# Optimization experiments

Measured on AMD Instinct MI355X. Metric: run time of the kernel, lower is better.

Reference implementation:

```python
import jax, jax.numpy as jnp
import numpy as np

B = 512          # number of (query, corpus) pairs
MAX_SET = 128    # max_set_size
D_IN, E_IN = 32, 16
D = 128          # node_state_dim == filters_3
E_ENC = 64
M_HID = 256
T_DIM = 128      # transform_dim
N_PROP = 5
SINKHORN_ITERS = 20
TEMP = 0.1
DEG = 8


def setup_inputs() -> dict:
    key = jax.random.key(0)
    ks = jax.random.split(key, 16)
    # alternating graph sizes: query 128/64, corpus 64/128
    qsizes = np.where(np.arange(B) % 2 == 0, 128, 64).astype(np.int32)
    csizes = np.where(np.arange(B) % 2 == 0, 64, 128).astype(np.int32)
    sizes_flat = np.stack([qsizes, csizes], 1).reshape(-1)        # [2B] interleaved q,c
    N = int(sizes_flat.sum())                                     # 98304
    E = DEG * N                                                   # 786432
    starts = np.concatenate([[0], np.cumsum(sizes_flat)[:-1]])
    graph_idx = np.repeat(np.arange(2 * B), sizes_flat).astype(np.int32)
    rng = np.random.default_rng(0)
    from_idx = rng.integers(0, N, E).astype(np.int64)
    g = graph_idx[from_idx]                                       # keep edges within a graph
    to_idx = (starts[g] + rng.integers(0, 1 << 30, E) % sizes_flat[g]).astype(np.int64)

    def W(k, shape):
        s = 1.0 / np.sqrt(shape[0])
        return jax.random.uniform(k, shape, jnp.float32, -s, s)

    return dict(
        node_features=jax.random.normal(ks[0], (N, D_IN), jnp.float32),
        edge_features=jax.random.normal(ks[1], (E, E_IN), jnp.float32),
        enc_node_w=W(ks[2], (D_IN, D)), enc_node_b=jnp.zeros((D,), jnp.float32),
        enc_edge_w=W(ks[3], (E_IN, E_ENC)), enc_edge_b=jnp.zeros((E_ENC,), jnp.float32),
        msg_w1=W(ks[4], (2 * D + E_ENC, M_HID)), msg_b1=jnp.zeros((M_HID,), jnp.float32),
        msg_w2=W(ks[5], (M_HID, D)), msg_b2=jnp.zeros((D,), jnp.float32),
        rmsg_w1=W(ks[6], (2 * D + E_ENC, M_HID)), rmsg_b1=jnp.zeros((M_HID,), jnp.float32),
        rmsg_w2=W(ks[7], (M_HID, D)), rmsg_b2=jnp.zeros((D,), jnp.float32),
        upd_w1=W(ks[8], (2 * D, M_HID)), upd_b1=jnp.zeros((M_HID,), jnp.float32),
        upd_w2=W(ks[9], (M_HID, D)), upd_b2=jnp.zeros((D,), jnp.float32),
        fc1_w=W(ks[10], (D, T_DIM)), fc1_b=jnp.zeros((T_DIM,), jnp.float32),
        fc2_w=W(ks[11], (T_DIM, T_DIM)), fc2_b=jnp.zeros((T_DIM,), jnp.float32),
        from_idx=jnp.asarray(from_idx, jnp.int32),
        to_idx=jnp.asarray(to_idx, jnp.int32),
        graph_idx=jnp.asarray(graph_idx, jnp.int32),
        qsizes=jnp.asarray(qsizes, jnp.int32),
        csizes=jnp.asarray(csizes, jnp.int32),
    )


def _mlp2(x, w1, b1, w2, b2):
    return jax.nn.relu(x @ w1 + b1) @ w2 + b2


def reference(node_features, edge_features, enc_node_w, enc_node_b, enc_edge_w, enc_edge_b,
              msg_w1, msg_b1, msg_w2, msg_b2, rmsg_w1, rmsg_b1, rmsg_w2, rmsg_b2,
              upd_w1, upd_b1, upd_w2, upd_b2, fc1_w, fc1_b, fc2_w, fc2_b,
              from_idx, to_idx, graph_idx, qsizes, csizes):
    N = node_features.shape[0]
    # GraphEncoder: linear MLPs on node / edge features
    h = node_features @ enc_node_w + enc_node_b                   # [N, D]
    e = edge_features @ enc_edge_w + enc_edge_b                   # [E, E_ENC]
    # GraphPropLayer applied n_prop_layers times (shared params)
    for _ in range(N_PROP):
        src, dst = h[from_idx], h[to_idx]
        m = _mlp2(jnp.concatenate([src, dst, e], -1), msg_w1, msg_b1, msg_w2, msg_b2)
        agg = jax.ops.segment_sum(m, to_idx, num_segments=N)
        mr = _mlp2(jnp.concatenate([dst, src, e], -1), rmsg_w1, rmsg_b1, rmsg_w2, rmsg_b2)
        agg = agg + jax.ops.segment_sum(mr, from_idx, num_segments=N)
        h = h + _mlp2(jnp.concatenate([agg, h], -1), upd_w1, upd_b1, upd_w2, upd_b2)
    # split into per-graph chunks and pad to MAX_SET (scatter by (pair, side, position))
    sizes_flat = jnp.stack([qsizes, csizes], 1).reshape(-1)       # [2B]
    starts = jnp.concatenate([jnp.zeros((1,), sizes_flat.dtype), jnp.cumsum(sizes_flat)[:-1]])
    pos = jnp.arange(N, dtype=jnp.int32) - starts[graph_idx]
    pair, side = graph_idx // 2, graph_idx % 2
    stacked = jnp.zeros((B, 2, MAX_SET, D), h.dtype).at[pair, side, pos].set(h)
    stacked_q, stacked_c = stacked[:, 0], stacked[:, 1]           # [B, MAX_SET, D]
    # masked transform
    tq = _mlp2(stacked_q, fc1_w, fc1_b, fc2_w, fc2_b)
    tc = _mlp2(stacked_c, fc1_w, fc1_b, fc2_w, fc2_b)
    ar = jnp.arange(MAX_SET)
    qmask = (ar[None, :] < qsizes[:, None]).astype(h.dtype)[:, :, None]
    cmask = (ar[None, :] < csizes[:, None]).astype(h.dtype)[:, :, None]
    mq, mc = qmask * tq, cmask * tc
    # sinkhorn (noise_factor = 0, temperature = 0.1, 20 iters)
    log_alpha = jnp.einsum('bqd,bcd->bqc', mq, mc) / TEMP         # [B, MAX_SET, MAX_SET]
    for _ in range(SINKHORN_ITERS):
        log_alpha = log_alpha - jax.scipy.special.logsumexp(log_alpha, axis=2, keepdims=True)
        log_alpha = log_alpha - jax.scipy.special.logsumexp(log_alpha, axis=1, keepdims=True)
    plan = jnp.exp(log_alpha)
    # masked residual score
    scores = -jnp.sum(jax.nn.relu(stacked_q - plan @ stacked_c), axis=(1, 2))  # [B]
    return scores
```

## Files before the change

### kernel.cpp

```cpp
#include <hip/hip_runtime.h>

using bf16x8 = __attribute__((ext_vector_type(8))) __bf16;
using u16x8  = __attribute__((ext_vector_type(8))) unsigned short;
using f32x4  = __attribute__((ext_vector_type(4))) float;
using f32x2  = __attribute__((ext_vector_type(2))) float;

#define DEV static __device__ __forceinline__

constexpr int NN = 98304;
constexpr int NE = 786432;
constexpr int NB = 512;

constexpr size_t OFF_HB  = 0;
constexpr size_t OFF_AGG = OFF_HB + (size_t)NN*128*2;
constexpr size_t OFF_TH  = OFF_AGG;
constexpr size_t OFF_TL  = OFF_AGG + (size_t)NN*128*2;
constexpr size_t OFF_W   = OFF_AGG + (size_t)NN*128*4;

constexpr size_t WO_W1TM = 0;
constexpr size_t WO_W1TR = WO_W1TM + (size_t)81920*2;
constexpr size_t WO_W2TM = WO_W1TR + (size_t)81920*2;
constexpr size_t WO_W2TR = WO_W2TM + (size_t)32768*2;
constexpr size_t WO_W1TU = WO_W2TR + (size_t)32768*2;
constexpr size_t WO_W2TU = WO_W1TU + (size_t)65536*2;
constexpr size_t WO_WNT  = WO_W2TU + (size_t)32768*2;
constexpr size_t WO_WETP = WO_WNT  + (size_t)4096*2;
constexpr size_t WO_FC1F = WO_WETP + (size_t)2048*2;
constexpr size_t WO_FC2F = WO_FC1F + (size_t)16384*4;
constexpr size_t WO_BNF  = WO_FC2F + (size_t)16384*4;
constexpr size_t WO_BEF  = WO_BNF + 128*4;
constexpr size_t WO_B1M  = WO_BEF + 64*4;
constexpr size_t WO_B2M  = WO_B1M + 256*4;
constexpr size_t WO_B1R  = WO_B2M + 128*4;
constexpr size_t WO_B2R  = WO_B1R + 256*4;
constexpr size_t WO_B1U  = WO_B2R + 128*4;
constexpr size_t WO_B2U  = WO_B1U + 256*4;
constexpr size_t WO_FC1B = WO_B2U + 128*4;
constexpr size_t WO_FC2B = WO_FC1B + 128*4;
constexpr size_t WO_FLAG = WO_FC2B + 128*4;
constexpr size_t WO_END  = WO_FLAG + 16;

constexpr size_t OFF_HL  = OFF_W + WO_END;
constexpr size_t WS_MINI = OFF_HL;
constexpr size_t WS_FULL = OFF_HL + (size_t)NN*128*2;

constexpr int    SCAN_CHUNKS= NN/256;
constexpr size_t CSR_INTS   = (size_t)2*(NN+1) + (size_t)2*NN + (size_t)2*NE + 768;
constexpr size_t CSR_BYTES  = CSR_INTS*4;
constexpr size_t WS_FULL_G  = WS_FULL + CSR_BYTES;
constexpr size_t WS_MINI_G  = WS_MINI + CSR_BYTES;

DEV unsigned short f2bf(float f){
  unsigned u = __float_as_uint(f);
  u += 0x7fffu + ((u >> 16) & 1u);
  return (unsigned short)(u >> 16);
}
DEV float bf2f(unsigned short s){ return __uint_as_float(((unsigned)s) << 16); }

DEV unsigned short ldbf(const void* p, size_t i, int fl){
  return fl ? ((const unsigned short*)p)[i] : f2bf(((const float*)p)[i]);
}
DEV float ldf(const void* p, size_t i, int fl){
  return fl ? bf2f(((const unsigned short*)p)[i]) : ((const float*)p)[i];
}

DEV f32x4 mfma16(u16x8 a, u16x8 b, f32x4 c){
  bf16x8 A, B;
  __builtin_memcpy(&A, &a, 16);
  __builtin_memcpy(&B, &b, 16);
  return __builtin_amdgcn_mfma_f32_16x16x32_bf16(A, B, c, 0, 0, 0);
}

__global__ void k_dtype(const unsigned short* nf_u16, int* flag){
  if (threadIdx.x != 0 || blockIdx.x != 0) return;
  int sane = 0;
  for (int i = 0; i < 64; ++i){
    unsigned short v = nf_u16[2*i];
    int e = (v >> 7) & 0xFF;
    if (e >= 0x70 && e <= 0x8E) sane++;
  }
  *flag = (sane >= 32) ? 1 : 0;
}

__global__ void k_sent(float* out){
  int i = blockIdx.x*256 + threadIdx.x;
  if (i < NB) out[i] = 10000.f;
}

__global__ void k_canary(void* out, const int* flag){
  int i = blockIdx.x*256 + threadIdx.x;
  if (i < NB){
    if (*flag) ((unsigned short*)out)[i] = (unsigned short)0x4580u;
    else       ((float*)out)[i] = 4096.f;
  }
}

__global__ void k_zero(float* agg){
  f32x4* p = (f32x4*)agg;
  int gtid = blockIdx.x*256 + threadIdx.x;
  for (int i = gtid; i < NN*128/4; i += 786432){
    f32x4 z = {0.f, 0.f, 0.f, 0.f};
    p[i] = z;
  }
}

__global__ void k_prep(
  const void* enc_node_w, const void* enc_node_b,
  const void* enc_edge_w, const void* enc_edge_b,
  const void* msg_w1, const void* msg_b1,
  const void* msg_w2, const void* msg_b2,
  const void* rmsg_w1, const void* rmsg_b1,
  const void* rmsg_w2, const void* rmsg_b2,
  const void* upd_w1, const void* upd_b1,
  const void* upd_w2, const void* upd_b2,
  const void* fc1_w, const void* fc1_b,
  const void* fc2_w, const void* fc2_b,
  char* wsb)
{
  int fl = *(const int*)(wsb + OFF_W + WO_FLAG);
  int i = blockIdx.x*256 + threadIdx.x;
  unsigned short* W1Tm = (unsigned short*)(wsb + OFF_W + WO_W1TM);
  unsigned short* W1Tr = (unsigned short*)(wsb + OFF_W + WO_W1TR);
  unsigned short* W2Tm = (unsigned short*)(wsb + OFF_W + WO_W2TM);
  unsigned short* W2Tr = (unsigned short*)(wsb + OFF_W + WO_W2TR);
  unsigned short* W1Tu = (unsigned short*)(wsb + OFF_W + WO_W1TU);
  unsigned short* W2Tu = (unsigned short*)(wsb + OFF_W + WO_W2TU);
  unsigned short* WnT  = (unsigned short*)(wsb + OFF_W + WO_WNT);
  unsigned short* WeTp = (unsigned short*)(wsb + OFF_W + WO_WETP);
  float* fc1f = (float*)(wsb + OFF_W + WO_FC1F);
  float* fc2f = (float*)(wsb + OFF_W + WO_FC2F);
  float* bnf  = (float*)(wsb + OFF_W + WO_BNF);
  float* bef  = (float*)(wsb + OFF_W + WO_BEF);
  float* b1m  = (float*)(wsb + OFF_W + WO_B1M);
  float* b2m  = (float*)(wsb + OFF_W + WO_B2M);
  float* b1r  = (float*)(wsb + OFF_W + WO_B1R);
  float* b2r  = (float*)(wsb + OFF_W + WO_B2R);
  float* b1u  = (float*)(wsb + OFF_W + WO_B1U);
  float* b2u  = (float*)(wsb + OFF_W + WO_B2U);
  float* f1b  = (float*)(wsb + OFF_W + WO_FC1B);
  float* f2b  = (float*)(wsb + OFF_W + WO_FC2B);

  if (i < 81920){ W1Tm[i] = ldbf(msg_w1,  (size_t)(i%320)*256 + (i/320), fl); return; } i -= 81920;
  if (i < 81920){ W1Tr[i] = ldbf(rmsg_w1, (size_t)(i%320)*256 + (i/320), fl); return; } i -= 81920;
  if (i < 32768){ W2Tm[i] = ldbf(msg_w2,  (size_t)(i%256)*128 + (i/256), fl); return; } i -= 32768;
  if (i < 32768){ W2Tr[i] = ldbf(rmsg_w2, (size_t)(i%256)*128 + (i/256), fl); return; } i -= 32768;
  if (i < 65536){ W1Tu[i] = ldbf(upd_w1,  (size_t)(i%256)*256 + (i/256), fl); return; } i -= 65536;
  if (i < 32768){ W2Tu[i] = ldbf(upd_w2,  (size_t)(i%256)*128 + (i/256), fl); return; } i -= 32768;
  if (i <  4096){ WnT[i]  = ldbf(enc_node_w, (size_t)(i%32)*128 + (i/32), fl); return; } i -= 4096;
  if (i <  2048){ int k = i%32, n = i/32;
                  WeTp[i] = (k<16) ? ldbf(enc_edge_w, (size_t)k*64 + n, fl) : (unsigned short)0; return; } i -= 2048;
  if (i < 16384){ fc1f[i] = ldf(fc1_w, i, fl); return; } i -= 16384;
  if (i < 16384){ fc2f[i] = ldf(fc2_w, i, fl); return; } i -= 16384;
  if (i <   128){ bnf[i] = ldf(enc_node_b, i, fl); return; } i -= 128;
  if (i <    64){ bef[i] = ldf(enc_edge_b, i, fl); return; } i -= 64;
  if (i <   256){ b1m[i] = ldf(msg_b1, i, fl); return; } i -= 256;
  if (i <   128){ b2m[i] = ldf(msg_b2, i, fl); return; } i -= 128;
  if (i <   256){ b1r[i] = ldf(rmsg_b1, i, fl); return; } i -= 256;
  if (i <   128){ b2r[i] = ldf(rmsg_b2, i, fl); return; } i -= 128;
  if (i <   256){ b1u[i] = ldf(upd_b1, i, fl); return; } i -= 256;
  if (i <   128){ b2u[i] = ldf(upd_b2, i, fl); return; } i -= 128;
  if (i <   128){ f1b[i] = ldf(fc1_b, i, fl); return; } i -= 128;
  if (i <   128){ f2b[i] = ldf(fc2_b, i, fl); return; }
}

__global__ void k_csr_zero(int* cur0, int* cur1){
  int i = blockIdx.x*256 + threadIdx.x;
  if (i < NN){ cur0[i] = 0; cur1[i] = 0; }
}
__global__ void k_csr_count(const int* from_idx, const int* to_idx, int* cur0, int* cur1){
  int e = blockIdx.x*256 + threadIdx.x;
  if (e < NE){
    atomicAdd(&cur0[to_idx[e]], 1);
    atomicAdd(&cur1[from_idx[e]], 1);
  }
}
__global__ void k_scan1(const int* cur0, const int* cur1, int* csum){
  __shared__ int red[256];
  int b = blockIdx.x, tid = threadIdx.x;
  const int* c = (b >= SCAN_CHUNKS) ? cur1 : cur0;
  int cb = (b >= SCAN_CHUNKS) ? (b - SCAN_CHUNKS) : b;
  red[tid] = c[cb*256 + tid];
  __syncthreads();
  for (int off = 128; off > 0; off >>= 1){
    if (tid < off) red[tid] += red[tid + off];
    __syncthreads();
  }
  if (tid == 0) csum[b] = red[0];
}
__global__ void k_scan2(int* csum, int* offs0, int* offs1){
  int wv = threadIdx.x >> 6, lane = threadIdx.x & 63;
  if (wv >= 2) return;
  int basei = wv * SCAN_CHUNKS;
  int carry = 0;
  for (int j = 0; j < SCAN_CHUNKS/64; ++j){
    int x = csum[basei + j*64 + lane];
    int s = x;
    for (int off = 1; off < 64; off <<= 1){
      int t = __shfl_up(s, off, 64);
      if (lane >= off) s += t;
    }
    csum[basei + j*64 + lane] = s - x + carry;
    carry += __shfl(s, 63, 64);
  }
  if (lane == 0){
    if (wv == 0) offs0[NN] = carry; else offs1[NN] = carry;
  }
}
__global__ void k_scan3(int* cur0, int* cur1, const int* csum, int* offs0, int* offs1){
  __shared__ int s[256];
  int b = blockIdx.x, tid = threadIdx.x;
  int dir = (b >= SCAN_CHUNKS) ? 1 : 0;
  int cb  = dir ? (b - SCAN_CHUNKS) : b;
  int* c    = dir ? cur1 : cur0;
  int* offs = dir ? offs1 : offs0;
  int v = c[cb*256 + tid];
  s[tid] = v;
  __syncthreads();
  for (int off = 1; off < 256; off <<= 1){
    int t = (tid >= off) ? s[tid - off] : 0;
    __syncthreads();
    s[tid] += t;
    __syncthreads();
  }
  int excl = s[tid] - v + csum[b];
  offs[cb*256 + tid] = excl;
  c[cb*256 + tid] = excl;
}
__global__ void k_csr_fill(const int* from_idx, const int* to_idx,
                           int* cur0, int* cur1, int* ent0, int* ent1){
  int e = blockIdx.x*256 + threadIdx.x;
  if (e < NE){
    int p0 = atomicAdd(&cur0[to_idx[e]], 1);   ent0[p0] = e;
    int p1 = atomicAdd(&cur1[from_idx[e]], 1); ent1[p1] = e;
  }
}

__global__ void __launch_bounds__(256) k_enc_node(
  const void* nf, const unsigned short* wnt, const float* bnf,
  unsigned short* hb, unsigned short* hl, int has_hl, const int* flag)
{
  int fl = *flag;
  const u16x8* wnt8 = (const u16x8*)wnt;
  int tid = threadIdx.x, wv = tid>>6, lane = tid&63, quad = lane>>4, l15 = lane&15;
  int n0 = blockIdx.x*64;
  f32x4 acc[4][2];
  for (int a=0;a<4;a++){ f32x4 z = {0.f,0.f,0.f,0.f}; acc[a][0]=z; acc[a][1]=z; }
  u16x8 av[4], bv[2];
  if (fl){
    const u16x8* nf8 = (const u16x8*)nf;
    for (int mt=0; mt<4; ++mt) av[mt] = nf8[(size_t)(n0 + mt*16 + l15)*4 + quad];
  } else {
    const float* nff = (const float*)nf;
    for (int mt=0; mt<4; ++mt){
      const float* rp = nff + (size_t)(n0 + mt*16 + l15)*32 + quad*8;
      u16x8 v;
      for (int j=0;j<8;j++) v[j] = f2bf(rp[j]);
      av[mt] = v;
    }
  }
  for (int nt=0; nt<2; ++nt) bv[nt] = wnt8[(size_t)(wv*32 + nt*16 + l15)*4 + quad];
  for (int mt=0; mt<4; ++mt)
    for (int nt=0; nt<2; ++nt)
      acc[mt][nt] = mfma16(av[mt], bv[nt], acc[mt][nt]);
  for (int mt=0; mt<4; ++mt)
    for (int nt=0; nt<2; ++nt){
      int n = wv*32 + nt*16 + l15;
      float bias = bnf[n];
      for (int r=0;r<4;r++){
        int m = mt*16 + quad*4 + r;
        float v = acc[mt][nt][r] + bias;
        size_t idx = (size_t)(n0+m)*128 + n;
        unsigned short hi = f2bf(v);
        hb[idx] = hi;
        if (has_hl) hl[idx] = f2bf(v - bf2f(hi));
      }
    }
}

__global__ void __launch_bounds__(256) k_msg(
  const unsigned short* hbg, const void* efg,
  const int* from_idx, const int* to_idx,
  const unsigned short* w1tm, const unsigned short* w1tr,
  const unsigned short* w2tm, const unsigned short* w2tr,
  const unsigned short* wetp, const float* bef,
  const float* b1m, const float* b2m, const float* b1r, const float* b2r,
  float* agg, const int* flag)
{
  __shared__ __align__(16) unsigned short XsB[40*32*8];
  __shared__ __align__(16) unsigned short HsB[32*32*8];
  __shared__ int fromS[32], toS[32];
  int fl = *flag;
  u16x8* Xs = (u16x8*)XsB;
  u16x8* Hs = (u16x8*)HsB;
  const u16x8* hb8   = (const u16x8*)hbg;
  const u16x8* wetp8 = (const u16x8*)wetp;
  const u16x8* w1tm8 = (const u16x8*)w1tm;
  const u16x8* w1tr8 = (const u16x8*)w1tr;
  const u16x8* w2tm8 = (const u16x8*)w2tm;
  const u16x8* w2tr8 = (const u16x8*)w2tr;

  int tid = threadIdx.x;
  int e0 = blockIdx.x*32;
  if (tid < 32) fromS[tid] = from_idx[e0 + tid];
  else if (tid < 64) toS[tid-32] = to_idx[e0 + tid - 32];
  __syncthreads();
  int m = tid & 31, g = tid >> 5;
  int wv = tid>>6, lane = tid&63, quad = lane>>4, l15 = lane&15;
  u16x8 zero8 = {0,0,0,0,0,0,0,0};

  for (int j=0; j<4; ++j){
    int kb = g + 8*j;
    u16x8 v = (kb < 16) ? hb8[(size_t)fromS[m]*16 + kb]
                        : hb8[(size_t)toS[m]*16 + (kb-16)];
    Xs[kb*32 + m] = v;
  }
  {
    f32x4 accE[2];
    for (int a=0;a<2;a++){ f32x4 z = {0.f,0.f,0.f,0.f}; accE[a]=z; }
    u16x8 bvE = wetp8[(size_t)(wv*16 + l15)*4 + quad];
    for (int mt=0; mt<2; ++mt){
      u16x8 avE = zero8;
      if (quad < 2){
        if (fl){
          avE = ((const u16x8*)efg)[(size_t)(e0 + mt*16 + l15)*2 + quad];
        } else {
          const float* ep = (const float*)efg + (size_t)(e0 + mt*16 + l15)*16 + quad*8;
          u16x8 v;
          for (int j=0;j<8;j++) v[j] = f2bf(ep[j]);
          avE = v;
        }
      }
      accE[mt] = mfma16(avE, bvE, accE[mt]);
    }
    int n = wv*16 + l15;
    float bias = bef[n];
    for (int mt=0; mt<2; ++mt)
      for (int r=0;r<4;r++){
        int me = mt*16 + quad*4 + r;
        XsB[((32 + (n>>3))*32 + me)*8 + (n&7)] = f2bf(accE[mt][r] + bias);
      }
  }
  __syncthreads();

  for (int dir=0; dir<2; ++dir){
    const u16x8* W1T = dir ? w1tr8 : w1tm8;
    const u16x8* W2T = dir ? w2tr8 : w2tm8;
    const float* B1  = dir ? b1r : b1m;
    const float* B2  = dir ? b2r : b2m;
    f32x4 acc1[2][4];
    for (int a=0;a<2;a++)
      for (int b=0;b<4;b++){ f32x4 z = {0.f,0.f,0.f,0.f}; acc1[a][b]=z; }
    for (int ks=0; ks<10; ++ks){
      u16x8 bv[4], av[2];
      for (int nt=0; nt<4; ++nt)
        bv[nt] = W1T[(size_t)(wv*64 + nt*16 + l15)*40 + ks*4 + quad];
      int kb = ks*4 + quad;
      int kbm = dir ? (kb < 32 ? (kb ^ 16) : kb) : kb;
      for (int mt=0; mt<2; ++mt)
        av[mt] = Xs[kbm*32 + mt*16 + l15];
      for (int mt=0; mt<2; ++mt)
        for (int nt=0; nt<4; ++nt)
          acc1[mt][nt] = mfma16(av[mt], bv[nt], acc1[mt][nt]);
    }
    __syncthreads();
    for (int mt=0; mt<2; ++mt)
      for (int nt=0; nt<4; ++nt){
        int n = wv*64 + nt*16 + l15;
        float bias = B1[n];
        for (int r=0;r<4;r++){
          int mm = mt*16 + quad*4 + r;
          float v = fmaxf(acc1[mt][nt][r] + bias, 0.f);
          HsB[((n>>3)*32 + mm)*8 + (n&7)] = f2bf(v);
        }
      }
    __syncthreads();
    f32x4 acc2[2][2];
    for (int a=0;a<2;a++)
      for (int b=0;b<2;b++){ f32x4 z = {0.f,0.f,0.f,0.f}; acc2[a][b]=z; }
    for (int ks=0; ks<8; ++ks){
      u16x8 bv[2], av[2];
      for (int nt=0; nt<2; ++nt)
        bv[nt] = W2T[(size_t)(wv*32 + nt*16 + l15)*32 + ks*4 + quad];
      for (int mt=0; mt<2; ++mt)
        av[mt] = Hs[(ks*4 + quad)*32 + mt*16 + l15];
      for (int mt=0; mt<2; ++mt)
        for (int nt=0; nt<2; ++nt)
          acc2[mt][nt] = mfma16(av[mt], bv[nt], acc2[mt][nt]);
    }
    for (int mt=0; mt<2; ++mt)
      for (int nt=0; nt<2; ++nt){
        int n = wv*32 + nt*16 + l15;
        float bias = B2[n];
        for (int r=0;r<4;r++){
          int mm = mt*16 + quad*4 + r;
          int row = dir ? fromS[mm] : toS[mm];
          atomicAdd(agg + (size_t)row*128 + n, acc2[mt][nt][r] + bias);
        }
      }
  }
}

__global__ void __launch_bounds__(512, 4) k_msg8(
  const unsigned short* hbg, const void* efg,
  const int* from_idx, const int* to_idx, const int* ent,
  const unsigned short* w1tm, const unsigned short* w1tr,
  const unsigned short* w2tm, const unsigned short* w2tr,
  const unsigned short* wetp, const float* bef,
  const float* b1m, const float* b2m, const float* b1r, const float* b2r,
  float* agg, const int* flag)
{
  __shared__ __align__(16) unsigned short XsB[40*64*8];
  __shared__ __align__(16) unsigned short HsB[32*64*8];
  __shared__ int eS[64], fromS[64], toS[64];
  __shared__ int runBeg[65];
  __shared__ int nRunsS;
  int fl = *flag;
  u16x8* Xs = (u16x8*)XsB;
  u16x8* Hs = (u16x8*)HsB;
  const u16x8* hb8   = (const u16x8*)hbg;
  const u16x8* wetp8 = (const u16x8*)wetp;
  const u16x8* w1tm8 = (const u16x8*)w1tm;
  const u16x8* w1tr8 = (const u16x8*)w1tr;
  const u16x8* w2tm8 = (const u16x8*)w2tm;
  const u16x8* w2tr8 = (const u16x8*)w2tr;

  int tid = threadIdx.x;
  int cpx = (int)gridDim.x >> 3;
  int bb = ((int)blockIdx.x & 7) * cpx + ((int)blockIdx.x >> 3);
  int e0 = bb * 64;
  if (tid < 64){
    int e = ent[e0 + tid];
    eS[tid] = e;
    fromS[tid] = from_idx[e];
    toS[tid]   = to_idx[e];
  }
  __syncthreads();
  int w = tid>>6, lane = tid&63, quad = lane>>4, l15 = lane&15;
  u16x8 zero8 = {0,0,0,0,0,0,0,0};

  if (tid == 0){
    int nr = 0;
    for (int mm=0; mm<64; ++mm)
      if (mm==0 || toS[mm]!=toS[mm-1]) runBeg[nr++] = mm;
    runBeg[nr] = 64; nRunsS = nr;
  }
  {
    int edge = tid & 63, cg = tid >> 6;
    for (int j=0; j<4; ++j){
      int kb = cg + 8*j;
      u16x8 v = (kb < 16) ? hb8[(size_t)fromS[edge]*16 + kb]
                          : hb8[(size_t)toS[edge]*16 + (kb-16)];
      Xs[kb*64 + edge] = v;
    }
  }
  {
    int wm = w >> 2, wn = w & 3;
    f32x4 accE[2];
    for (int a=0;a<2;a++){ f32x4 z = {0.f,0.f,0.f,0.f}; accE[a]=z; }
    u16x8 bvE = wetp8[(size_t)(wn*16 + l15)*4 + quad];
    for (int mt=0; mt<2; ++mt){
      u16x8 avE = zero8;
      if (quad < 2){
        int e = eS[wm*32 + mt*16 + l15];
        if (fl){
          avE = ((const u16x8*)efg)[(size_t)e*2 + quad];
        } else {
          const float* ep = (const float*)efg + (size_t)e*16 + quad*8;
          u16x8 v;
          for (int j=0;j<8;j++) v[j] = f2bf(ep[j]);
          avE = v;
        }
      }
      accE[mt] = mfma16(avE, bvE, accE[mt]);
    }
    int n = wn*16 + l15;
    float bias = bef[n];
    for (int mt=0; mt<2; ++mt)
      for (int r=0;r<4;r++){
        int me = wm*32 + mt*16 + quad*4 + r;
        XsB[((32 + (n>>3))*64 + me)*8 + (n&7)] = f2bf(accE[mt][r] + bias);
      }
  }
  __syncthreads();

  for (int dir=0; dir<2; ++dir){
    const u16x8* W1T = dir ? w1tr8 : w1tm8;
    const u16x8* W2T = dir ? w2tr8 : w2tm8;
    const float* B1  = dir ? b1r : b1m;
    f32x4 acc1[4][2];
    for (int a=0;a<4;a++)
      for (int b=0;b<2;b++){ f32x4 z = {0.f,0.f,0.f,0.f}; acc1[a][b]=z; }
    u16x8 bvA[2], bvB[2];
    for (int nt=0; nt<2; ++nt)
      bvA[nt] = W1T[(size_t)(w*32 + nt*16 + l15)*40 + quad];
    for (int ks=0; ks<10; ++ks){
      if (ks < 9)
        for (int nt=0; nt<2; ++nt)
          bvB[nt] = W1T[(size_t)(w*32 + nt*16 + l15)*40 + (ks+1)*4 + quad];
      else { bvB[0] = bvA[0]; bvB[1] = bvA[1]; }
      int kb = ks*4 + quad;
      int kbm = dir ? (kb < 32 ? (kb ^ 16) : kb) : kb;
      u16x8 av[4];
      for (int mt=0; mt<4; ++mt)
        av[mt] = Xs[kbm*64 + mt*16 + l15];
      for (int mt=0; mt<4; ++mt)
        for (int nt=0; nt<2; ++nt)
          acc1[mt][nt] = mfma16(av[mt], bvA[nt], acc1[mt][nt]);
      bvA[0] = bvB[0]; bvA[1] = bvB[1];
    }
    if (dir == 1) __syncthreads();
    for (int mt=0; mt<4; ++mt)
      for (int nt=0; nt<2; ++nt){
        int n = w*32 + nt*16 + l15;
        float bias = B1[n];
        for (int r=0;r<4;r++){
          int mm = mt*16 + quad*4 + r;
          float v = fmaxf(acc1[mt][nt][r] + bias, 0.f);
          HsB[((n>>3)*64 + mm)*8 + (n&7)] = f2bf(v);
        }
      }
    __syncthreads();
    f32x4 acc2[4];
    for (int a=0;a<4;a++){ f32x4 z = {0.f,0.f,0.f,0.f}; acc2[a]=z; }
    int n2 = w*16 + l15;
    u16x8 bvC = W2T[(size_t)n2*32 + quad];
    for (int ks=0; ks<8; ++ks){
      u16x8 bvN = bvC;
      if (ks < 7) bvN = W2T[(size_t)n2*32 + (ks+1)*4 + quad];
      u16x8 av[4];
      for (int mt=0; mt<4; ++mt)
        av[mt] = Hs[(ks*4 + quad)*64 + mt*16 + l15];
      for (int mt=0; mt<4; ++mt)
        acc2[mt] = mfma16(av[mt], bvC, acc2[mt]);
      bvC = bvN;
    }
    if (dir == 0){
      __syncthreads();
      float* P = (float*)HsB;
      float bias = b2m[n2];
      for (int mt=0; mt<4; ++mt)
        for (int r=0;r<4;r++){
          int mm = mt*16 + quad*4 + r;
          P[mm*128 + n2] = acc2[mt][r] + bias;
        }
      __syncthreads();
      int col = tid & 127, grp = tid >> 7;
      int nr = nRunsS;
      for (int k = grp; k < nr; k += 4){
        int r0 = runBeg[k], r1 = runBeg[k+1];
        float s = 0.f;
        for (int mm = r0; mm < r1; ++mm) s += P[mm*128 + col];
        atomicAdd(agg + (size_t)toS[r0]*128 + col, s);
      }
    } else {
      float bias = b2r[n2];
      for (int mt=0; mt<4; ++mt)
        for (int r=0;r<4;r++){
          int mm = mt*16 + quad*4 + r;
          atomicAdd(agg + (size_t)fromS[mm]*128 + n2, acc2[mt][r] + bias);
        }
    }
  }
}

__global__ void __launch_bounds__(512, 4) k_upd(
  float* agg, const unsigned short* hbg,
  const unsigned short* w1tu, const unsigned short* w2tu,
  const float* b1u, const float* b2u,
  unsigned short* hb, unsigned short* hl, int has_hl)
{
  __shared__ __align__(16) unsigned short XsB[32*64*8];
  __shared__ __align__(16) unsigned short HsB[32*64*8];
  u16x8* Xs = (u16x8*)XsB;
  u16x8* Hs = (u16x8*)HsB;
  const u16x8* hb8   = (const u16x8*)hbg;
  const u16x8* w1tu8 = (const u16x8*)w1tu;
  const u16x8* w2tu8 = (const u16x8*)w2tu;
  int tid = threadIdx.x;
  int n0 = blockIdx.x*64;
  {
    int node = tid & 63, cg = tid >> 6;
    for (int j=0; j<4; ++j){
      int kb = cg + 8*j;
      u16x8 v;
      if (kb < 16){
        const float* ap = agg + (size_t)(n0+node)*128 + kb*8;
        for (int t=0;t<8;t++) v[t] = f2bf(ap[t]);
      } else {
        v = hb8[(size_t)(n0+node)*16 + (kb-16)];
      }
      Xs[kb*64 + node] = v;
    }
  }
  __syncthreads();
  {
    f32x4* ap4 = (f32x4*)(agg + (size_t)n0*128);
    f32x4 z = {0.f,0.f,0.f,0.f};
    for (int i = tid; i < 64*128/4; i += 512) ap4[i] = z;
  }
  int w = tid>>6, lane = tid&63, quad = lane>>4, l15 = lane&15;
  f32x4 acc1[4][2];
  for (int a=0;a<4;a++)
    for (int b=0;b<2;b++){ f32x4 z = {0.f,0.f,0.f,0.f}; acc1[a][b]=z; }
  {
    u16x8 bvA[2], bvB[2];
    for (int nt=0; nt<2; ++nt)
      bvA[nt] = w1tu8[(size_t)(w*32 + nt*16 + l15)*32 + quad];
    for (int ks=0; ks<8; ++ks){
      if (ks < 7)
        for (int nt=0; nt<2; ++nt)
          bvB[nt] = w1tu8[(size_t)(w*32 + nt*16 + l15)*32 + (ks+1)*4 + quad];
      else { bvB[0] = bvA[0]; bvB[1] = bvA[1]; }
      u16x8 av[4];
      for (int mt=0; mt<4; ++mt)
        av[mt] = Xs[(ks*4 + quad)*64 + mt*16 + l15];
      for (int mt=0; mt<4; ++mt)
        for (int nt=0; nt<2; ++nt)
          acc1[mt][nt] = mfma16(av[mt], bvA[nt], acc1[mt][nt]);
      bvA[0] = bvB[0]; bvA[1] = bvB[1];
    }
  }
  __syncthreads();
  for (int mt=0; mt<4; ++mt)
    for (int nt=0; nt<2; ++nt){
      int n = w*32 + nt*16 + l15;
      float bias = b1u[n];
      for (int r=0;r<4;r++){
        int mm = mt*16 + quad*4 + r;
        float v = fmaxf(acc1[mt][nt][r] + bias, 0.f);
        HsB[((n>>3)*64 + mm)*8 + (n&7)] = f2bf(v);
      }
    }
  __syncthreads();
  f32x4 acc2[4];
  for (int a=0;a<4;a++){ f32x4 z = {0.f,0.f,0.f,0.f}; acc2[a]=z; }
  int n2 = w*16 + l15;
  {
    u16x8 bvC = w2tu8[(size_t)n2*32 + quad];
    for (int ks=0; ks<8; ++ks){
      u16x8 bvN = bvC;
      if (ks < 7) bvN = w2tu8[(size_t)n2*32 + (ks+1)*4 + quad];
      u16x8 av[4];
      for (int mt=0; mt<4; ++mt)
        av[mt] = Hs[(ks*4 + quad)*64 + mt*16 + l15];
      for (int mt=0; mt<4; ++mt)
        acc2[mt] = mfma16(av[mt], bvC, acc2[mt]);
      bvC = bvN;
    }
  }
  float bias = b2u[n2];
  for (int mt=0; mt<4; ++mt)
    for (int r=0;r<4;r++){
      int mm = mt*16 + quad*4 + r;
      size_t idx = (size_t)(n0+mm)*128 + n2;
      float base = bf2f(hb[idx]);
      if (has_hl) base += bf2f(hl[idx]);
      float nv = base + acc2[mt][r] + bias;
      unsigned short hi = f2bf(nv);
      hb[idx] = hi;
      if (has_hl) hl[idx] = f2bf(nv - bf2f(hi));
    }
}

__global__ void __launch_bounds__(256) k_tmlp(
  const unsigned short* hb, const unsigned short* hl, int has_hl,
  const float* fc1f, const float* fc2f,
  const float* fc1b, const float* fc2b, unsigned short* Th, unsigned short* Tl)
{
  __shared__ float Xs[16][128];
  __shared__ float Hsm[16][128];
  int tid = threadIdx.x, wv = tid>>6, lane = tid&63;
  int nodeBase = blockIdx.x*16 + wv*4;
  for (int i=0;i<4;i++){
    size_t base = (size_t)(nodeBase+i)*128 + lane*2;
    float x0 = bf2f(hb[base]), x1 = bf2f(hb[base+1]);
    if (has_hl){ x0 += bf2f(hl[base]); x1 += bf2f(hl[base+1]); }
    Xs[wv*4+i][lane*2] = x0; Xs[wv*4+i][lane*2+1] = x1;
  }
  __syncthreads();
  float a0[4], a1[4];
  for (int i=0;i<4;i++){ a0[i] = fc1b[lane*2]; a1[i] = fc1b[lane*2+1]; }
  for (int k=0;k<128;k++){
    f32x2 w = *(const f32x2*)&fc1f[k*128 + lane*2];
    for (int i=0;i<4;i++){ float x = Xs[wv*4+i][k]; a0[i] += x*w[0]; a1[i] += x*w[1]; }
  }
  for (int i=0;i<4;i++){
    Hsm[wv*4+i][lane*2]   = fmaxf(a0[i], 0.f);
    Hsm[wv*4+i][lane*2+1] = fmaxf(a1[i], 0.f);
  }
  __syncthreads();
  for (int i=0;i<4;i++){ a0[i] = fc2b[lane*2]; a1[i] = fc2b[lane*2+1]; }
  for (int k=0;k<128;k++){
    f32x2 w = *(const f32x2*)&fc2f[k*128 + lane*2];
    for (int i=0;i<4;i++){ float x = Hsm[wv*4+i][k]; a0[i] += x*w[0]; a1[i] += x*w[1]; }
  }
  for (int i=0;i<4;i++){
    size_t idx = (size_t)(nodeBase+i)*128 + lane*2;
    float t0 = a0[i], t1 = a1[i];
    unsigned short h0 = f2bf(t0), h1 = f2bf(t1);
    Th[idx] = h0; Th[idx+1] = h1;
    Tl[idx]   = f2bf(t0 - bf2f(h0));
    Tl[idx+1] = f2bf(t1 - bf2f(h1));
  }
}

__global__ void __launch_bounds__(256) k_pair(
  const unsigned short* Th, const unsigned short* Tl,
  const unsigned short* hb, const unsigned short* hl, int has_hl,
  void* outv, const int* flag)
{
  __shared__ float la[8448];
  __shared__ float red[4];
  const u16x8* th8 = (const u16x8*)Th;
  const u16x8* tl8 = (const u16x8*)Tl;
  int b = blockIdx.x;
  int even = ((b & 1) == 0);
  int qs = even ? 128 : 64;
  int cs = 192 - qs;
  int nr = even ? 128 : 65;
  int nc = even ? 65 : 128;
  int st = nc + 1;
  int q0 = 192*b, c0 = q0 + qs;
  int tid = threadIdx.x, wv = tid>>6, lane = tid&63, quad = lane>>4, l15 = lane&15;
  u16x8 zero8 = {0,0,0,0,0,0,0,0};

  f32x4 acc[2][8];
  for (int a=0;a<2;a++)
    for (int c=0;c<8;c++){ f32x4 z = {0.f,0.f,0.f,0.f}; acc[a][c]=z; }
  for (int pass=0; pass<3; ++pass){
    const u16x8* A  = (pass==2) ? tl8 : th8;
    const u16x8* Bm = (pass==1) ? tl8 : th8;
    for (int ks=0; ks<4; ++ks){
      u16x8 av[2], bv[8];
      for (int mt=0; mt<2; ++mt){
        int q = wv*32 + mt*16 + l15;
        av[mt] = (q < qs) ? A[(size_t)(q0+q)*16 + ks*4 + quad] : zero8;
      }
      for (int nt=0; nt<8; ++nt){
        int c = nt*16 + l15;
        bv[nt] = (c < cs) ? Bm[(size_t)(c0+c)*16 + ks*4 + quad] : zero8;
      }
      for (int mt=0; mt<2; ++mt)
        for (int nt=0; nt<8; ++nt)
          acc[mt][nt] = mfma16(av[mt], bv[nt], acc[mt][nt]);
    }
  }
  for (int mt=0; mt<2; ++mt)
    for (int nt=0; nt<8; ++nt)
      for (int r=0;r<4;r++){
        int q = wv*32 + mt*16 + quad*4 + r;
        int c = nt*16 + l15;
        if (q < nr && c < nc) la[q*st + c] = acc[mt][nt][r] * 10.0f;
      }
  __syncthreads();

  for (int it=0; it<20; ++it){
    if (tid < nr){
      float* row = &la[tid*st];
      float mx = -1e30f;
      for (int c=0;c<nc;c++) mx = fmaxf(mx, row[c]);
      float s = 0.f, last = 0.f;
      for (int c=0;c<nc;c++){ float e = __expf(row[c]-mx); s += e; last = e; }
      if (even) s += 63.f * last;
      float l = mx + __logf(s);
      for (int c=0;c<nc;c++) row[c] -= l;
    }
    __syncthreads();
    if (tid < nc){
      int c = tid;
      float mx = -1e30f;
      for (int r=0;r<nr;r++) mx = fmaxf(mx, la[r*st + c]);
      float s = 0.f, last = 0.f;
      for (int r=0;r<nr;r++){ float e = __expf(la[r*st + c]-mx); s += e; last = e; }
      if (!even) s += 63.f * last;
      float l = mx + __logf(s);
      for (int r=0;r<nr;r++) la[r*st + c] -= l;
    }
    __syncthreads();
  }
  for (int i = tid; i < 8448; i += 256) la[i] = __expf(la[i]);
  __syncthreads();

  int d = tid & 127, qg = tid >> 7;
  int nsweep = (nr + 15) >> 4;
  float partial = 0.f;
  for (int sweep=0; sweep<nsweep; ++sweep){
    int qb = sweep*16 + qg*8;
    float acc2[8];
    for (int j=0;j<8;j++) acc2[j] = 0.f;
    for (int c=0; c<cs; ++c){
      size_t si = (size_t)(c0+c)*128 + d;
      float s = bf2f(hb[si]);
      if (has_hl) s += bf2f(hl[si]);
      for (int j=0;j<8;j++){
        int r = qb + j;
        if (r < nr) acc2[j] += la[r*st + c] * s;
      }
    }
    for (int j=0;j<8;j++){
      int r = qb + j;
      if (r < nr){
        float w = (!even && r == 64) ? 64.f : 1.f;
        float sq = 0.f;
        if (r < qs){
          size_t si = (size_t)(q0+r)*128 + d;
          sq = bf2f(hb[si]);
          if (has_hl) sq += bf2f(hl[si]);
        }
        partial += w * fmaxf(sq - acc2[j], 0.f);
      }
    }
  }
  for (int off=32; off>0; off>>=1) partial += __shfl_down(partial, off, 64);
  if (lane == 0) red[wv] = partial;
  __syncthreads();
  if (tid == 0){
    float tot = red[0] + red[1] + red[2] + red[3];
    if (*flag) ((unsigned short*)outv)[b] = f2bf(-tot);
    else       ((float*)outv)[b] = -tot;
  }
}

extern "C" void kernel_launch(void* const* d_in, const int* in_sizes, int n_in,
                              void* d_out, int out_size, void* d_ws, size_t ws_size,
                              hipStream_t stream)
{
  if (ws_size < WS_MINI){
    k_sent<<<2, 256, 0, stream>>>((float*)d_out);
    return;
  }
  int has_hl = 0, use_s8 = 0;
  size_t off_csr = 0;
  if (ws_size >= WS_FULL_G){ has_hl = 1; use_s8 = 1; off_csr = WS_FULL; }
  else if (ws_size >= WS_FULL){ has_hl = 1; use_s8 = 0; }
  else if (ws_size >= WS_MINI_G){ has_hl = 0; use_s8 = 1; off_csr = WS_MINI; }

  const int* from_idx = (const int*)d_in[22];
  const int* to_idx   = (const int*)d_in[23];

  char* wsb = (char*)d_ws;
  unsigned short* hb  = (unsigned short*)(wsb + OFF_HB);
  unsigned short* hl  = (unsigned short*)(wsb + OFF_HL);
  float* agg          = (float*)(wsb + OFF_AGG);
  unsigned short* Th  = (unsigned short*)(wsb + OFF_TH);
  unsigned short* Tl  = (unsigned short*)(wsb + OFF_TL);
  int* flag           = (int*)(wsb + OFF_W + WO_FLAG);

  const unsigned short* w1tm = (const unsigned short*)(wsb + OFF_W + WO_W1TM);
  const unsigned short* w1tr = (const unsigned short*)(wsb + OFF_W + WO_W1TR);
  const unsigned short* w2tm = (const unsigned short*)(wsb + OFF_W + WO_W2TM);
  const unsigned short* w2tr = (const unsigned short*)(wsb + OFF_W + WO_W2TR);
  const unsigned short* w1tu = (const unsigned short*)(wsb + OFF_W + WO_W1TU);
  const unsigned short* w2tu = (const unsigned short*)(wsb + OFF_W + WO_W2TU);
  const unsigned short* wnt  = (const unsigned short*)(wsb + OFF_W + WO_WNT);
  const unsigned short* wetp = (const unsigned short*)(wsb + OFF_W + WO_WETP);
  const float* fc1f  = (const float*)(wsb + OFF_W + WO_FC1F);
  const float* fc2f  = (const float*)(wsb + OFF_W + WO_FC2F);
  const float* bnf   = (const float*)(wsb + OFF_W + WO_BNF);
  const float* bef   = (const float*)(wsb + OFF_W + WO_BEF);
  const float* b1m   = (const float*)(wsb + OFF_W + WO_B1M);
  const float* b2m   = (const float*)(wsb + OFF_W + WO_B2M);
  const float* b1r   = (const float*)(wsb + OFF_W + WO_B1R);
  const float* b2r   = (const float*)(wsb + OFF_W + WO_B2R);
  const float* b1u   = (const float*)(wsb + OFF_W + WO_B1U);
  const float* b2u   = (const float*)(wsb + OFF_W + WO_B2U);
  const float* f1b   = (const float*)(wsb + OFF_W + WO_FC1B);
  const float* f2b   = (const float*)(wsb + OFF_W + WO_FC2B);

  int* offs0 = (int*)(wsb + off_csr);
  int* offs1 = offs0 + (NN + 1);
  int* cur0  = offs1 + (NN + 1);
  int* cur1  = cur0 + NN;
  int* ent0  = cur1 + NN;
  int* ent1  = ent0 + NE;
  int* csum  = ent1 + NE;

  k_dtype<<<1, 64, 0, stream>>>((const unsigned short*)d_in[0], flag);

  k_canary<<<2, 256, 0, stream>>>(d_out, flag);

  k_prep<<<1439, 256, 0, stream>>>(
    d_in[2],  d_in[3],  d_in[4],  d_in[5],
    d_in[6],  d_in[7],  d_in[8],  d_in[9],
    d_in[10], d_in[11], d_in[12], d_in[13],
    d_in[14], d_in[15], d_in[16], d_in[17],
    d_in[18], d_in[19], d_in[20], d_in[21],
    wsb);

  if (use_s8){
    k_csr_zero <<<NN/256, 256, 0, stream>>>(cur0, cur1);
    k_csr_count<<<NE/256, 256, 0, stream>>>(from_idx, to_idx, cur0, cur1);
    k_scan1    <<<2*SCAN_CHUNKS, 256, 0, stream>>>(cur0, cur1, csum);
    k_scan2    <<<1, 128, 0, stream>>>(csum, offs0, offs1);
    k_scan3    <<<2*SCAN_CHUNKS, 256, 0, stream>>>(cur0, cur1, csum, offs0, offs1);
    k_csr_fill <<<NE/256, 256, 0, stream>>>(from_idx, to_idx, cur0, cur1, ent0, ent1);
  }

  k_enc_node<<<NN/64, 256, 0, stream>>>(d_in[0], wnt, bnf, hb, hl, has_hl, flag);

  k_zero<<<3072, 256, 0, stream>>>(agg);
  for (int r=0; r<5; ++r){
    if (use_s8){
      k_msg8<<<NE/64, 512, 0, stream>>>(hb, d_in[1],
          from_idx, to_idx, ent0, w1tm, w1tr, w2tm, w2tr, wetp, bef,
          b1m, b2m, b1r, b2r, agg, flag);
    } else {
      k_msg<<<NE/32, 256, 0, stream>>>(hb, d_in[1],
          from_idx, to_idx, w1tm, w1tr, w2tm, w2tr, wetp, bef,
          b1m, b2m, b1r, b2r, agg, flag);
    }
    k_upd<<<NN/64, 512, 0, stream>>>(agg, hb, w1tu, w2tu, b1u, b2u, hb, hl, has_hl);
  }

  k_tmlp<<<NN/16, 256, 0, stream>>>(hb, hl, has_hl, fc1f, fc2f, f1b, f2b, Th, Tl);
  k_pair<<<NB, 256, 0, stream>>>(Th, Tl, hb, hl, has_hl, d_out, flag);
}
```

Baseline: 5.816 ms.

## Process reverse messages with a second destination-sorted edge order for segmented reduction

The message kernel now runs two passes per block. The first uses edges sorted by destination, the second uses edges sorted by source (ent1). Each pass gathers its own node features and edge encodings, so the reverse direction can also use run-length segmented sums before atomics instead of one atomic per element. This trades fewer, coalesced-by-run atomics on the reverse path for a second gather of node rows and edge features plus recomputing the edge encoder. Manual software prefetch of weight fragments in the message and update GEMM loops is also removed in favour of simple per-iteration loads.

```diff
diff --git a/kernel.cpp b/kernel.cpp
--- a/kernel.cpp
+++ b/kernel.cpp
@@ -400,9 +400,10 @@
   }
 }
 
-__global__ void __launch_bounds__(512, 4) k_msg8(
+__global__ void __launch_bounds__(512, 4) k_msg11(
   const unsigned short* hbg, const void* efg,
-  const int* from_idx, const int* to_idx, const int* ent,
+  const int* from_idx, const int* to_idx,
+  const int* ent0, const int* ent1,
   const unsigned short* w1tm, const unsigned short* w1tr,
   const unsigned short* w2tm, const unsigned short* w2tr,
   const unsigned short* wetp, const float* bef,
@@ -411,7 +412,7 @@
 {
   __shared__ __align__(16) unsigned short XsB[40*64*8];
   __shared__ __align__(16) unsigned short HsB[32*64*8];
-  __shared__ int eS[64], fromS[64], toS[64];
+  __shared__ int eS[64], oS[64], tS[64];
   __shared__ int runBeg[65];
   __shared__ int nRunsS;
   int fl = *flag;
@@ -428,87 +429,85 @@
   int cpx = (int)gridDim.x >> 3;
   int bb = ((int)blockIdx.x & 7) * cpx + ((int)blockIdx.x >> 3);
   int e0 = bb * 64;
-  if (tid < 64){
-    int e = ent[e0 + tid];
-    eS[tid] = e;
-    fromS[tid] = from_idx[e];
-    toS[tid]   = to_idx[e];
-  }
-  __syncthreads();
   int w = tid>>6, lane = tid&63, quad = lane>>4, l15 = lane&15;
   u16x8 zero8 = {0,0,0,0,0,0,0,0};
 
-  if (tid == 0){
-    int nr = 0;
-    for (int mm=0; mm<64; ++mm)
-      if (mm==0 || toS[mm]!=toS[mm-1]) runBeg[nr++] = mm;
-    runBeg[nr] = 64; nRunsS = nr;
-  }
-  {
-    int edge = tid & 63, cg = tid >> 6;
-    for (int j=0; j<4; ++j){
-      int kb = cg + 8*j;
-      u16x8 v = (kb < 16) ? hb8[(size_t)fromS[edge]*16 + kb]
-                          : hb8[(size_t)toS[edge]*16 + (kb-16)];
-      Xs[kb*64 + edge] = v;
-    }
-  }
-  {
-    int wm = w >> 2, wn = w & 3;
-    f32x4 accE[2];
-    for (int a=0;a<2;a++){ f32x4 z = {0.f,0.f,0.f,0.f}; accE[a]=z; }
-    u16x8 bvE = wetp8[(size_t)(wn*16 + l15)*4 + quad];
-    for (int mt=0; mt<2; ++mt){
-      u16x8 avE = zero8;
-      if (quad < 2){
-        int e = eS[wm*32 + mt*16 + l15];
-        if (fl){
-          avE = ((const u16x8*)efg)[(size_t)e*2 + quad];
-        } else {
-          const float* ep = (const float*)efg + (size_t)e*16 + quad*8;
-          u16x8 v;
-          for (int j=0;j<8;j++) v[j] = f2bf(ep[j]);
-          avE = v;
+  for (int part = 0; part < 2; ++part){
+    const int* ent   = part ? ent1 : ent0;
+    const int* oidx  = part ? to_idx : from_idx;
+    const int* tidx  = part ? from_idx : to_idx;
+    const u16x8* W1T = part ? w1tr8 : w1tm8;
+    const u16x8* W2T = part ? w2tr8 : w2tm8;
+    const float* B1  = part ? b1r : b1m;
+    const float* B2  = part ? b2r : b2m;
+
+    __syncthreads();
+    if (tid < 64){
+      int e = ent[e0 + tid];
+      eS[tid] = e;
+      oS[tid] = oidx[e];
+      tS[tid] = tidx[e];
+    }
+    __syncthreads();
+    if (tid == 0){
+      int nr = 0;
+      for (int mm=0; mm<64; ++mm)
+        if (mm==0 || tS[mm]!=tS[mm-1]) runBeg[nr++] = mm;
+      runBeg[nr] = 64; nRunsS = nr;
+    }
+    {
+      int edge = tid & 63, cg = tid >> 6;
+      for (int j=0; j<4; ++j){
+        int kb = cg + 8*j;
+        u16x8 v = (kb < 16) ? hb8[(size_t)oS[edge]*16 + kb]
+                            : hb8[(size_t)tS[edge]*16 + (kb-16)];
+        Xs[kb*64 + edge] = v;
+      }
+    }
+    {
+      int wm = w >> 2, wn = w & 3;
+      f32x4 accE[2];
+      for (int a=0;a<2;a++){ f32x4 z = {0.f,0.f,0.f,0.f}; accE[a]=z; }
+      u16x8 bvE = wetp8[(size_t)(wn*16 + l15)*4 + quad];
+      for (int mt=0; mt<2; ++mt){
+        u16x8 avE = zero8;
+        if (quad < 2){
+          int e = eS[wm*32 + mt*16 + l15];
+          if (fl){
+            avE = ((const u16x8*)efg)[(size_t)e*2 + quad];
+          } else {
+            const float* ep = (const float*)efg + (size_t)e*16 + quad*8;
+            u16x8 v;
+            for (int j=0;j<8;j++) v[j] = f2bf(ep[j]);
+            avE = v;
+          }
         }
-      }
-      accE[mt] = mfma16(avE, bvE, accE[mt]);
-    }
-    int n = wn*16 + l15;
-    float bias = bef[n];
-    for (int mt=0; mt<2; ++mt)
-      for (int r=0;r<4;r++){
-        int me = wm*32 + mt*16 + quad*4 + r;
-        XsB[((32 + (n>>3))*64 + me)*8 + (n&7)] = f2bf(accE[mt][r] + bias);
-      }
-  }
-  __syncthreads();
-
-  for (int dir=0; dir<2; ++dir){
-    const u16x8* W1T = dir ? w1tr8 : w1tm8;
-    const u16x8* W2T = dir ? w2tr8 : w2tm8;
-    const float* B1  = dir ? b1r : b1m;
+        accE[mt] = mfma16(avE, bvE, accE[mt]);
+      }
+      int n = wn*16 + l15;
+      float bias = bef[n];
+      for (int mt=0; mt<2; ++mt)
+        for (int r=0;r<4;r++){
+          int me = wm*32 + mt*16 + quad*4 + r;
+          XsB[((32 + (n>>3))*64 + me)*8 + (n&7)] = f2bf(accE[mt][r] + bias);
+        }
+    }
+    __syncthreads();
+
     f32x4 acc1[4][2];
     for (int a=0;a<4;a++)
       for (int b=0;b<2;b++){ f32x4 z = {0.f,0.f,0.f,0.f}; acc1[a][b]=z; }
-    u16x8 bvA[2], bvB[2];
-    for (int nt=0; nt<2; ++nt)
-      bvA[nt] = W1T[(size_t)(w*32 + nt*16 + l15)*40 + quad];
     for (int ks=0; ks<10; ++ks){
-      if (ks < 9)
-        for (int nt=0; nt<2; ++nt)
-          bvB[nt] = W1T[(size_t)(w*32 + nt*16 + l15)*40 + (ks+1)*4 + quad];
-      else { bvB[0] = bvA[0]; bvB[1] = bvA[1]; }
+      u16x8 bv[2], av[4];
+      for (int nt=0; nt<2; ++nt)
+        bv[nt] = W1T[(size_t)(w*32 + nt*16 + l15)*40 + ks*4 + quad];
       int kb = ks*4 + quad;
-      int kbm = dir ? (kb < 32 ? (kb ^ 16) : kb) : kb;
-      u16x8 av[4];
       for (int mt=0; mt<4; ++mt)
-        av[mt] = Xs[kbm*64 + mt*16 + l15];
+        av[mt] = Xs[kb*64 + mt*16 + l15];
       for (int mt=0; mt<4; ++mt)
         for (int nt=0; nt<2; ++nt)
-          acc1[mt][nt] = mfma16(av[mt], bvA[nt], acc1[mt][nt]);
-      bvA[0] = bvB[0]; bvA[1] = bvB[1];
-    }
-    if (dir == 1) __syncthreads();
+          acc1[mt][nt] = mfma16(av[mt], bv[nt], acc1[mt][nt]);
+    }
     for (int mt=0; mt<4; ++mt)
       for (int nt=0; nt<2; ++nt){
         int n = w*32 + nt*16 + l15;
@@ -523,42 +522,34 @@
     f32x4 acc2[4];
     for (int a=0;a<4;a++){ f32x4 z = {0.f,0.f,0.f,0.f}; acc2[a]=z; }
     int n2 = w*16 + l15;
-    u16x8 bvC = W2T[(size_t)n2*32 + quad];
     for (int ks=0; ks<8; ++ks){
-      u16x8 bvN = bvC;
-      if (ks < 7) bvN = W2T[(size_t)n2*32 + (ks+1)*4 + quad];
+      u16x8 bv1 = W2T[(size_t)n2*32 + ks*4 + quad];
       u16x8 av[4];
       for (int mt=0; mt<4; ++mt)
         av[mt] = Hs[(ks*4 + quad)*64 + mt*16 + l15];
       for (int mt=0; mt<4; ++mt)
-        acc2[mt] = mfma16(av[mt], bvC, acc2[mt]);
-      bvC = bvN;
-    }
-    if (dir == 0){
-      __syncthreads();
-      float* P = (float*)HsB;
-      float bias = b2m[n2];
+        acc2[mt] = mfma16(av[mt], bv1, acc2[mt]);
+    }
+    __syncthreads();
+    float* P = (float*)HsB;
+    {
+      float bias = B2[n2];
       for (int mt=0; mt<4; ++mt)
         for (int r=0;r<4;r++){
           int mm = mt*16 + quad*4 + r;
           P[mm*128 + n2] = acc2[mt][r] + bias;
         }
-      __syncthreads();
+    }
+    __syncthreads();
+    {
       int col = tid & 127, grp = tid >> 7;
       int nr = nRunsS;
       for (int k = grp; k < nr; k += 4){
         int r0 = runBeg[k], r1 = runBeg[k+1];
         float s = 0.f;
         for (int mm = r0; mm < r1; ++mm) s += P[mm*128 + col];
-        atomicAdd(agg + (size_t)toS[r0]*128 + col, s);
-      }
-    } else {
-      float bias = b2r[n2];
-      for (int mt=0; mt<4; ++mt)
-        for (int r=0;r<4;r++){
-          int mm = mt*16 + quad*4 + r;
-          atomicAdd(agg + (size_t)fromS[mm]*128 + n2, acc2[mt][r] + bias);
-        }
+        atomicAdd(agg + (size_t)tS[r0]*128 + col, s);
+      }
     }
   }
 }
@@ -602,23 +593,15 @@
   f32x4 acc1[4][2];
   for (int a=0;a<4;a++)
     for (int b=0;b<2;b++){ f32x4 z = {0.f,0.f,0.f,0.f}; acc1[a][b]=z; }
-  {
-    u16x8 bvA[2], bvB[2];
+  for (int ks=0; ks<8; ++ks){
+    u16x8 bv[2], av[4];
     for (int nt=0; nt<2; ++nt)
-      bvA[nt] = w1tu8[(size_t)(w*32 + nt*16 + l15)*32 + quad];
-    for (int ks=0; ks<8; ++ks){
-      if (ks < 7)
-        for (int nt=0; nt<2; ++nt)
-          bvB[nt] = w1tu8[(size_t)(w*32 + nt*16 + l15)*32 + (ks+1)*4 + quad];
-      else { bvB[0] = bvA[0]; bvB[1] = bvA[1]; }
-      u16x8 av[4];
-      for (int mt=0; mt<4; ++mt)
-        av[mt] = Xs[(ks*4 + quad)*64 + mt*16 + l15];
-      for (int mt=0; mt<4; ++mt)
-        for (int nt=0; nt<2; ++nt)
-          acc1[mt][nt] = mfma16(av[mt], bvA[nt], acc1[mt][nt]);
-      bvA[0] = bvB[0]; bvA[1] = bvB[1];
-    }
+      bv[nt] = w1tu8[(size_t)(w*32 + nt*16 + l15)*32 + ks*4 + quad];
+    for (int mt=0; mt<4; ++mt)
+      av[mt] = Xs[(ks*4 + quad)*64 + mt*16 + l15];
+    for (int mt=0; mt<4; ++mt)
+      for (int nt=0; nt<2; ++nt)
+        acc1[mt][nt] = mfma16(av[mt], bv[nt], acc1[mt][nt]);
   }
   __syncthreads();
   for (int mt=0; mt<4; ++mt)
@@ -635,18 +618,13 @@
   f32x4 acc2[4];
   for (int a=0;a<4;a++){ f32x4 z = {0.f,0.f,0.f,0.f}; acc2[a]=z; }
   int n2 = w*16 + l15;
-  {
-    u16x8 bvC = w2tu8[(size_t)n2*32 + quad];
-    for (int ks=0; ks<8; ++ks){
-      u16x8 bvN = bvC;
-      if (ks < 7) bvN = w2tu8[(size_t)n2*32 + (ks+1)*4 + quad];
-      u16x8 av[4];
-      for (int mt=0; mt<4; ++mt)
-        av[mt] = Hs[(ks*4 + quad)*64 + mt*16 + l15];
-      for (int mt=0; mt<4; ++mt)
-        acc2[mt] = mfma16(av[mt], bvC, acc2[mt]);
-      bvC = bvN;
-    }
+  for (int ks=0; ks<8; ++ks){
+    u16x8 bv2 = w2tu8[(size_t)n2*32 + ks*4 + quad];
+    u16x8 av[4];
+    for (int mt=0; mt<4; ++mt)
+      av[mt] = Hs[(ks*4 + quad)*64 + mt*16 + l15];
+    for (int mt=0; mt<4; ++mt)
+      acc2[mt] = mfma16(av[mt], bv2, acc2[mt]);
   }
   float bias = b2u[n2];
   for (int mt=0; mt<4; ++mt)
@@ -829,11 +807,11 @@
     k_sent<<<2, 256, 0, stream>>>((float*)d_out);
     return;
   }
-  int has_hl = 0, use_s8 = 0;
+  int has_hl = 0, use_s = 0;
   size_t off_csr = 0;
-  if (ws_size >= WS_FULL_G){ has_hl = 1; use_s8 = 1; off_csr = WS_FULL; }
-  else if (ws_size >= WS_FULL){ has_hl = 1; use_s8 = 0; }
-  else if (ws_size >= WS_MINI_G){ has_hl = 0; use_s8 = 1; off_csr = WS_MINI; }
+  if (ws_size >= WS_FULL_G){ has_hl = 1; use_s = 1; off_csr = WS_FULL; }
+  else if (ws_size >= WS_FULL){ has_hl = 1; use_s = 0; }
+  else if (ws_size >= WS_MINI_G){ has_hl = 0; use_s = 1; off_csr = WS_MINI; }
 
   const int* from_idx = (const int*)d_in[22];
   const int* to_idx   = (const int*)d_in[23];
@@ -887,7 +865,7 @@
     d_in[18], d_in[19], d_in[20], d_in[21],
     wsb);
 
-  if (use_s8){
+  if (use_s){
     k_csr_zero <<<NN/256, 256, 0, stream>>>(cur0, cur1);
     k_csr_count<<<NE/256, 256, 0, stream>>>(from_idx, to_idx, cur0, cur1);
     k_scan1    <<<2*SCAN_CHUNKS, 256, 0, stream>>>(cur0, cur1, csum);
@@ -900,9 +878,10 @@
 
   k_zero<<<3072, 256, 0, stream>>>(agg);
   for (int r=0; r<5; ++r){
-    if (use_s8){
-      k_msg8<<<NE/64, 512, 0, stream>>>(hb, d_in[1],
-          from_idx, to_idx, ent0, w1tm, w1tr, w2tm, w2tr, wetp, bef,
+    if (use_s){
+      k_msg11<<<NE/64, 512, 0, stream>>>(hb, d_in[1],
+          from_idx, to_idx, ent0, ent1,
+          w1tm, w1tr, w2tm, w2tr, wetp, bef,
           b1m, b2m, b1r, b2r, agg, flag);
     } else {
       k_msg<<<NE/32, 256, 0, stream>>>(hb, d_in[1],
```

After: 6.181 ms. 6.3% more time.
